# Kernel optimization log

Hardware: AMD Instinct MI355X
Metric: run time of the kernel (lower is better)

The kernel has to match this reference:

```python
import jax, jax.numpy as jnp
import numpy as np

B, L, DIM, H = 2, 2048, 2048, 16
D = DIM // H  # head_dim = 128
EPS = 1e-6


def _rope_freqs(seq_len: int, head_dim: int, theta: float = 10000.0) -> jnp.ndarray:
    # Flux-style rotation matrix: [1, 1, L, D/2, 2, 2]
    pos = np.arange(seq_len, dtype=np.float32)
    inv = 1.0 / (theta ** (np.arange(0, head_dim, 2, dtype=np.float32) / head_dim))
    ang = np.einsum('l,d->ld', pos, inv)  # [L, D/2]
    cos, sin = np.cos(ang), np.sin(ang)
    rot = np.stack([np.stack([cos, -sin], -1), np.stack([sin, cos], -1)], -2)  # [L, D/2, 2, 2]
    return jnp.asarray(rot[None, None])


def _rms_norm(x, scale):
    rrms = jax.lax.rsqrt(jnp.mean(jnp.square(x), axis=-1, keepdims=True) + EPS)
    return x * rrms * scale


def _apply_rope(xq, xk, freqs_cis):
    # xq/xk: [B, H, L, D]; freqs_cis: [1, 1, L, D/2, 2, 2]
    def rot(x):
        xr = x.reshape(*x.shape[:-1], -1, 1, 2)  # [B,H,L,D/2,1,2]
        out = freqs_cis[..., 0] * xr[..., 0] + freqs_cis[..., 1] * xr[..., 1]
        return out.reshape(x.shape)
    return rot(xq), rot(xk)


def setup_inputs() -> dict:
    key = jax.random.key(0)
    ks = jax.random.split(key, 4)
    x = jax.random.normal(ks[0], (B, L, DIM), dtype=jnp.float32)
    qkv_w = jax.random.normal(ks[1], (DIM, 3 * DIM), dtype=jnp.float32) * 0.02
    qkv_b = jnp.zeros((3 * DIM,), dtype=jnp.float32)
    q_scale = jnp.ones((D,), dtype=jnp.float32)
    k_scale = jnp.ones((D,), dtype=jnp.float32)
    proj_w = jax.random.normal(ks[2], (DIM, DIM), dtype=jnp.float32) * 0.02
    proj_b = jnp.zeros((DIM,), dtype=jnp.float32)
    pe = _rope_freqs(L, D)
    return {"x": x, "pe": pe, "qkv_w": qkv_w, "qkv_b": qkv_b,
            "q_scale": q_scale, "k_scale": k_scale,
            "proj_w": proj_w, "proj_b": proj_b}


def reference(x, pe, qkv_w, qkv_b, q_scale, k_scale, proj_w, proj_b):
    b, l, _ = x.shape
    qkv = x @ qkv_w + qkv_b                      # [B, L, 3*DIM]
    qkv = qkv.reshape(b, l, 3, H, D)
    qkv = jnp.transpose(qkv, (2, 0, 3, 1, 4))    # [3, B, H, L, D]
    q, k, v = qkv[0], qkv[1], qkv[2]
    q = _rms_norm(q, q_scale)
    k = _rms_norm(k, k_scale)
    q, k = _apply_rope(q, k, pe)
    scores = jnp.einsum('bhqd,bhkd->bhqk', q, k) / jnp.sqrt(jnp.float32(D))
    attn = jax.nn.softmax(scores, axis=-1)
    o = jnp.einsum('bhqk,bhkd->bhqd', attn, v)   # [B, H, L, D]
    o = jnp.transpose(o, (0, 2, 1, 3)).reshape(b, l, H * D)
    return o @ proj_w + proj_b
```

## Files before the change

### kernel.cpp

```cpp
#include <hip/hip_runtime.h>
#include <cstdint>
#include <cstddef>

#define BB 2
#define HB 16
#define LL 2048
#define DD 128
#define MM 4096
#define KK 2048
#define N1 6144
#define N2 2048
#define BHLD (BB*HB*LL*DD)

typedef unsigned short u16;
typedef __bf16 bf16x8 __attribute__((ext_vector_type(8)));
typedef short  s16x4  __attribute__((ext_vector_type(4)));
typedef float  f32x4  __attribute__((ext_vector_type(4)));

typedef __attribute__((address_space(1))) void* as1_ptr;
typedef __attribute__((address_space(3))) void* as3_ptr;

__device__ __forceinline__ void gload16(const void* g, void* l) {
  __builtin_amdgcn_global_load_lds((as1_ptr)g, (as3_ptr)l, 16, 0, 0);
}

__device__ __forceinline__ float bf2f(u16 u) {
  union { unsigned v; float f; } c; c.v = ((unsigned)u) << 16; return c.f;
}
__device__ __forceinline__ u16 f2bf(float f) {
  unsigned u = __builtin_bit_cast(unsigned, f);
  return (u16)((u + 0x7FFFu + ((u >> 16) & 1u)) >> 16);
}


__global__ __launch_bounds__(256) void f32_to_bf16_vec(
    const float* __restrict__ in, u16* __restrict__ out, int n4) {
  int i = blockIdx.x * 256 + threadIdx.x;
  if (i >= n4) return;
  float4 v = ((const float4*)in)[i];
  ushort4 o;
  o.x = f2bf(v.x); o.y = f2bf(v.y); o.z = f2bf(v.z); o.w = f2bf(v.w);
  ((ushort4*)out)[i] = o;
}

__global__ __launch_bounds__(256) void transpose_f32_bf16(
    const float* __restrict__ in, u16* __restrict__ out, int R, int C) {
  __shared__ float t[32][33];
  int c0 = blockIdx.x * 32, r0 = blockIdx.y * 32;
  int tx = threadIdx.x & 31, ty = threadIdx.x >> 5;
#pragma unroll
  for (int i = ty; i < 32; i += 8)
    t[i][tx] = in[(size_t)(r0 + i) * C + c0 + tx];
  __syncthreads();
#pragma unroll
  for (int i = ty; i < 32; i += 8)
    out[(size_t)(c0 + i) * R + r0 + tx] = f2bf(t[tx][i]);
}

template<int MODE>
__global__ __launch_bounds__(256) void gemm_bt(
    const u16* __restrict__ A, const u16* __restrict__ Bt,
    const float* __restrict__ bias, void* __restrict__ Cout,
    int Msz, int Nsz, int Ksz)
{
  __shared__ __align__(16) u16 As[128*64];
  __shared__ __align__(16) u16 Bs[128*64];
  const int tid  = threadIdx.x;
  const int lane = tid & 63;
  const int wid  = tid >> 6;
  const int l15  = lane & 15, quad = lane >> 4;
  const int m0 = blockIdx.y * 128, n0 = blockIdx.x * 128;
  const int wm = (wid >> 1) * 64, wn = (wid & 1) * 64;

  f32x4 acc[4][4] = {};

  for (int ks = 0; ks < Ksz; ks += 64) {
    __syncthreads();
#pragma unroll
    for (int j = 0; j < 4; j++) {
      const int s = (wid*4 + j)*64 + lane;
      const int row = s >> 3, pc = (s & 7) ^ (row & 7);
      gload16(&A [(size_t)(m0 + row) * Ksz + ks + pc*8], &As[(wid*4 + j)*512]);
      gload16(&Bt[(size_t)(n0 + row) * Ksz + ks + pc*8], &Bs[(wid*4 + j)*512]);
    }
    __syncthreads();
#pragma unroll
    for (int kh = 0; kh < 2; kh++) {
      bf16x8 af[4], bfr[4];
#pragma unroll
      for (int i = 0; i < 4; i++) {
        const int r = wm + i*16 + l15;
        af[i]  = *(const bf16x8*)&As[r*64 + (((kh*4 + quad) ^ (r & 7)))*8];
      }
#pragma unroll
      for (int i = 0; i < 4; i++) {
        const int r = wn + i*16 + l15;
        bfr[i] = *(const bf16x8*)&Bs[r*64 + (((kh*4 + quad) ^ (r & 7)))*8];
      }
#pragma unroll
      for (int i = 0; i < 4; i++)
#pragma unroll
        for (int j = 0; j < 4; j++)
          acc[i][j] = __builtin_amdgcn_mfma_f32_16x16x32_bf16(af[i], bfr[j], acc[i][j], 0, 0, 0);
    }
  }

#pragma unroll
  for (int i = 0; i < 4; i++) {
#pragma unroll
    for (int j = 0; j < 4; j++) {
      const int col = n0 + wn + j*16 + l15;
      const float bv = bias[col];
#pragma unroll
      for (int r = 0; r < 4; r++) {
        const int row = m0 + wm + i*16 + quad*4 + r;
        float v = acc[i][j][r] + bv;
        if (MODE == 0) {
          u16* qkv = (u16*)Cout;
          int t = col >> 11, hd = col & 2047, h = hd >> 7, d = hd & 127;
          int b = row >> 11, l = row & (LL - 1);
          size_t dst;
          if (t < 2) dst = (size_t)t * BHLD + (((size_t)(b*HB + h)) * LL + l) * DD + d;
          else       dst = (size_t)2 * BHLD + (((size_t)(b*HB + h)) * DD + d) * LL + l;
          qkv[dst] = f2bf(v);
        } else {
          ((float*)Cout)[(size_t)row * Nsz + col] = v;
        }
      }
    }
  }
}

__global__ __launch_bounds__(256) void norm_rope(
    u16* __restrict__ qkv, const float* __restrict__ pe,
    const float* __restrict__ qsc, const float* __restrict__ ksc)
{
  const int wid = threadIdx.x >> 6, lane = threadIdx.x & 63;
  const int r = blockIdx.x * 4 + wid;
  const int l = r & (LL - 1);
  const float4 p4 = *(const float4*)&pe[((size_t)l * 64 + lane) * 4];
#pragma unroll
  for (int t = 0; t < 2; t++) {
    u16* base = qkv + (size_t)t * BHLD + (size_t)r * DD + lane * 2;
    const float* sc = t ? ksc : qsc;
    ushort2 xx = *(const ushort2*)base;
    float x0 = bf2f(xx.x), x1 = bf2f(xx.y);
    float ss = x0*x0 + x1*x1;
#pragma unroll
    for (int m = 1; m < 64; m <<= 1) ss += __shfl_xor(ss, m, 64);
    float rr = rsqrtf(ss * (1.0f/128.0f) + 1e-6f);
    if (t == 0) rr *= 0.08838834764831845f;
    float y0 = x0 * rr * sc[lane*2], y1 = x1 * rr * sc[lane*2 + 1];
    ushort2 oo;
    oo.x = f2bf(p4.x * y0 + p4.y * y1);
    oo.y = f2bf(p4.z * y0 + p4.w * y1);
    *(ushort2*)base = oo;
  }
}

#define BKT 64
__global__ __launch_bounds__(256, 2) void attn(
    const u16* __restrict__ qkv, u16* __restrict__ Oout)
{
  __shared__ __align__(16) u16 Ksh[2][BKT * DD];
  __shared__ __align__(16) u16 Vsh[2][DD * BKT];

  const int bh = blockIdx.x >> 4, qt = blockIdx.x & 15;
  const int wid = threadIdx.x >> 6, lane = threadIdx.x & 63;
  const int l15 = lane & 15, quad = lane >> 4;
  const int q0 = qt * 128 + wid * 32;
  const u16* qp = qkv + (size_t)bh * LL * DD;
  const u16* kp = qkv + (size_t)BHLD + (size_t)bh * LL * DD;
  const u16* vp = qkv + (size_t)2 * BHLD + (size_t)bh * DD * LL;

  bf16x8 qb[2][4];
#pragma unroll
  for (int qf = 0; qf < 2; qf++)
#pragma unroll
    for (int f = 0; f < 4; f++)
      qb[qf][f] = *(const bf16x8*)&qp[(size_t)(q0 + qf*16 + l15) * DD + f*32 + quad*8];

  float l_acc[2] = {0.f, 0.f};
  f32x4 oacc[2][8] = {};

  auto stage = [&](int buf, int k0) {
#pragma unroll
    for (int j = 0; j < 4; j++) {
      const int s = (wid*4 + j)*64 + lane;
      {
        const int r = s >> 4, c = s & 15;
        const int lc = (c & 8) | ((c & 7) ^ (r & 7));
        gload16(&kp[(size_t)(k0 + r) * DD + lc*8], &Ksh[buf][(wid*4 + j)*512]);
      }
      {
        const int r = s >> 3, c = s & 7;
        const int lc = c ^ (r & 7);
        gload16(&vp[(size_t)r * LL + k0 + lc*8], &Vsh[buf][(wid*4 + j)*512]);
      }
    }
  };

  stage(0, 0);
  int cur = 0;

  for (int k0 = 0; k0 < LL; k0 += BKT) {
    __syncthreads();
    if (k0 + BKT < LL) stage(cur ^ 1, k0 + BKT);

    f32x4 s[2][4] = {};
#pragma unroll
    for (int f = 0; f < 4; f++) {
      bf16x8 kf[4];
#pragma unroll
      for (int mt = 0; mt < 4; mt++) {
        const int rr = mt*16 + l15;
        const int Lc = f*4 + quad;
        const int pc = (Lc & 8) | ((Lc & 7) ^ (rr & 7));
        kf[mt] = *(const bf16x8*)&Ksh[cur][rr*DD + pc*8];
      }
#pragma unroll
      for (int qf = 0; qf < 2; qf++)
#pragma unroll
        for (int mt = 0; mt < 4; mt++)
          s[qf][mt] = __builtin_amdgcn_mfma_f32_16x16x32_bf16(kf[mt], qb[qf][f], s[qf][mt], 0, 0, 0);
    }

    s16x4 pa[2][4];
#pragma unroll
    for (int qf = 0; qf < 2; qf++) {
#pragma unroll
      for (int mt = 0; mt < 4; mt++) {
        float p0 = __expf(s[qf][mt][0] - 12.f);
        float p1 = __expf(s[qf][mt][1] - 12.f);
        float p2 = __expf(s[qf][mt][2] - 12.f);
        float p3 = __expf(s[qf][mt][3] - 12.f);
        l_acc[qf] += (p0 + p1) + (p2 + p3);
        pa[qf][mt][0] = (short)f2bf(p0); pa[qf][mt][1] = (short)f2bf(p1);
        pa[qf][mt][2] = (short)f2bf(p2); pa[qf][mt][3] = (short)f2bf(p3);
      }
    }

#pragma unroll
    for (int t = 0; t < 4; t++) {
      s16x4 vb[8];
#pragma unroll
      for (int c = 0; c < 8; c++) {
        const int rv = c*16 + l15;
        const int pc = (t*2 + (quad >> 1)) ^ (l15 & 7);
        vb[c] = *(const s16x4*)&Vsh[cur][rv*BKT + pc*8 + (quad & 1)*4];
      }
#pragma unroll
      for (int qf = 0; qf < 2; qf++)
#pragma unroll
        for (int c = 0; c < 8; c++)
          oacc[qf][c] = __builtin_amdgcn_mfma_f32_16x16x16bf16_1k(pa[qf][t], vb[c], oacc[qf][c], 0, 0, 0);
    }
    cur ^= 1;
  }

#pragma unroll
  for (int qf = 0; qf < 2; qf++) {
    l_acc[qf] += __shfl_xor(l_acc[qf], 16, 64);
    l_acc[qf] += __shfl_xor(l_acc[qf], 32, 64);
  }
  const int b = bh >> 4, h = bh & 15;
#pragma unroll
  for (int qf = 0; qf < 2; qf++) {
    float lr[4];
#pragma unroll
    for (int r = 0; r < 4; r++)
      lr[r] = 1.0f / __shfl(l_acc[qf], (quad << 4) | (quad*4 + r), 64);
#pragma unroll
    for (int c = 0; c < 8; c++)
#pragma unroll
      for (int r = 0; r < 4; r++) {
        int qrow = q0 + qf*16 + quad*4 + r;
        Oout[((size_t)(b*LL + qrow)) * N2 + h*DD + c*16 + l15] = f2bf(oacc[qf][c][r] * lr[r]);
      }
  }
}


extern "C" void kernel_launch(void* const* d_in, const int* in_sizes, int n_in,
                              void* d_out, int out_size, void* d_ws, size_t ws_size,
                              hipStream_t stream) {
  const float* x       = (const float*)d_in[0];
  const float* pe      = (const float*)d_in[1];
  const float* qkv_w   = (const float*)d_in[2];
  const float* qkv_b   = (const float*)d_in[3];
  const float* q_scale = (const float*)d_in[4];
  const float* k_scale = (const float*)d_in[5];
  const float* proj_w  = (const float*)d_in[6];
  const float* proj_b  = (const float*)d_in[7];

  char* ws = (char*)d_ws;
  u16* xb   = (u16*)(ws + 0);
  u16* w1t  = (u16*)(ws + 16777216);
  u16* w2t  = (u16*)(ws + 41943040);
  u16* qkv  = (u16*)(ws + 50331648);
  u16* attO = (u16*)(ws + 100663296);

  f32_to_bf16_vec<<<(MM*KK/4)/256, 256, 0, stream>>>(x, xb, MM*KK/4);
  transpose_f32_bf16<<<dim3(N1/32, KK/32), 256, 0, stream>>>(qkv_w, w1t, KK, N1);
  transpose_f32_bf16<<<dim3(N2/32, KK/32), 256, 0, stream>>>(proj_w, w2t, KK, N2);
  gemm_bt<0><<<dim3(N1/128, MM/128), 256, 0, stream>>>(xb, w1t, qkv_b, (void*)qkv, MM, N1, KK);
  norm_rope<<<(BB*HB*LL)/4, 256, 0, stream>>>(qkv, pe, q_scale, k_scale);
  attn<<<BB*HB*(LL/128), 256, 0, stream>>>(qkv, attO);
  gemm_bt<1><<<dim3(N2/128, MM/128), 256, 0, stream>>>(attO, w2t, proj_b, d_out, MM, N2, KK);
}
```

Measured before the change: 435.6 us.

## Replace GEMM with 256x256 double-buffered 8-wave pipelined kernel

Replaces the 128x128 single-buffered bf16 GEMM with a 256x256 tile, 512-thread kernel that double-buffers A/B in LDS and interleaves global-to-LDS loads with MFMA phases, using barriers, waitcnt and setprio. It also remaps workgroup indices with a swizzle so neighbouring blocks are spread out, aimed at L2 locality. The goal is to hide global load latency and raise data reuse per block. In exchange it uses 128KB of LDS per block and many more accumulator registers. The 2048x2048 projection GEMM then has only 128 blocks, which may underfill the GPU.

```diff
diff --git a/kernel.cpp b/kernel.cpp
--- a/kernel.cpp
+++ b/kernel.cpp
@@ -57,72 +57,133 @@
     out[(size_t)(c0 + i) * R + r0 + tx] = f2bf(t[tx][i]);
 }
 
+
+#define PH_ENTER \
+  __builtin_amdgcn_s_barrier(); \
+  asm volatile("s_waitcnt lgkmcnt(0)" ::: "memory"); \
+  __builtin_amdgcn_sched_barrier(0); \
+  __builtin_amdgcn_s_setprio(1);
+#define PH_EXIT \
+  __builtin_amdgcn_s_setprio(0); \
+  __builtin_amdgcn_s_barrier();
+#define PH_EXIT_VM \
+  __builtin_amdgcn_s_setprio(0); \
+  asm volatile("s_waitcnt vmcnt(4)" ::: "memory"); \
+  __builtin_amdgcn_s_barrier();
+
+#define QUAD_MFMA(MB, NB) \
+  { _Pragma("unroll") for (int mm = 0; mm < 4; mm++) \
+    _Pragma("unroll") for (int nn = 0; nn < 2; nn++) { \
+      acc[(MB)+mm][(NB)+nn] = __builtin_amdgcn_mfma_f32_16x16x32_bf16(af[mm][0], bfr[(NB)+nn][0], acc[(MB)+mm][(NB)+nn], 0, 0, 0); \
+      acc[(MB)+mm][(NB)+nn] = __builtin_amdgcn_mfma_f32_16x16x32_bf16(af[mm][1], bfr[(NB)+nn][1], acc[(MB)+mm][(NB)+nn], 0, 0, 0); \
+    } }
+
+#define LOAD_A4(BSEL, MH) \
+  { _Pragma("unroll") for (int mm = 0; mm < 4; mm++) \
+    _Pragma("unroll") for (int ks = 0; ks < 2; ks++) { \
+      const int r_ = wr*128 + ((MH)*4 + mm)*16 + l15; \
+      af[mm][ks] = *(const bf16x8*)&As[BSEL][r_*64 + (((ks*4 + quad) ^ (r_ & 7)) << 3)]; \
+    } }
+#define LOAD_B2(BSEL, NB) \
+  { _Pragma("unroll") for (int nn = 0; nn < 2; nn++) \
+    _Pragma("unroll") for (int ks = 0; ks < 2; ks++) { \
+      const int r_ = wc*64 + ((NB) + nn)*16 + l15; \
+      bfr[(NB)+nn][ks] = *(const bf16x8*)&Bs[BSEL][r_*64 + (((ks*4 + quad) ^ (r_ & 7)) << 3)]; \
+    } }
+
 template<int MODE>
-__global__ __launch_bounds__(256) void gemm_bt(
-    const u16* __restrict__ A, const u16* __restrict__ Bt,
+__global__ __launch_bounds__(512, 2) void gemm256(
+    const u16* __restrict__ Ag, const u16* __restrict__ Bg,
     const float* __restrict__ bias, void* __restrict__ Cout,
     int Msz, int Nsz, int Ksz)
 {
-  __shared__ __align__(16) u16 As[128*64];
-  __shared__ __align__(16) u16 Bs[128*64];
+  __shared__ __align__(16) u16 As[2][256*64];
+  __shared__ __align__(16) u16 Bs[2][256*64];
+
   const int tid  = threadIdx.x;
   const int lane = tid & 63;
   const int wid  = tid >> 6;
   const int l15  = lane & 15, quad = lane >> 4;
-  const int m0 = blockIdx.y * 128, n0 = blockIdx.x * 128;
-  const int wm = (wid >> 1) * 64, wn = (wid & 1) * 64;
-
-  f32x4 acc[4][4] = {};
-
-  for (int ks = 0; ks < Ksz; ks += 64) {
-    __syncthreads();
-#pragma unroll
-    for (int j = 0; j < 4; j++) {
-      const int s = (wid*4 + j)*64 + lane;
-      const int row = s >> 3, pc = (s & 7) ^ (row & 7);
-      gload16(&A [(size_t)(m0 + row) * Ksz + ks + pc*8], &As[(wid*4 + j)*512]);
-      gload16(&Bt[(size_t)(n0 + row) * Ksz + ks + pc*8], &Bs[(wid*4 + j)*512]);
-    }
-    __syncthreads();
-#pragma unroll
-    for (int kh = 0; kh < 2; kh++) {
-      bf16x8 af[4], bfr[4];
-#pragma unroll
-      for (int i = 0; i < 4; i++) {
-        const int r = wm + i*16 + l15;
-        af[i]  = *(const bf16x8*)&As[r*64 + (((kh*4 + quad) ^ (r & 7)))*8];
-      }
-#pragma unroll
-      for (int i = 0; i < 4; i++) {
-        const int r = wn + i*16 + l15;
-        bfr[i] = *(const bf16x8*)&Bs[r*64 + (((kh*4 + quad) ^ (r & 7)))*8];
-      }
-#pragma unroll
-      for (int i = 0; i < 4; i++)
-#pragma unroll
-        for (int j = 0; j < 4; j++)
-          acc[i][j] = __builtin_amdgcn_mfma_f32_16x16x32_bf16(af[i], bfr[j], acc[i][j], 0, 0, 0);
-    }
-  }
-
-#pragma unroll
-  for (int i = 0; i < 4; i++) {
-#pragma unroll
-    for (int j = 0; j < 4; j++) {
-      const int col = n0 + wn + j*16 + l15;
+  const int wr   = wid >> 2, wc = wid & 3;
+
+  const int nwg = gridDim.x * gridDim.y;
+  const int lin = blockIdx.y * gridDim.x + blockIdx.x;
+  const int swz = (lin & 7) * (nwg >> 3) + (lin >> 3);
+  const int bn0 = (swz % gridDim.x) * 256;
+  const int bm0 = (swz / gridDim.x) * 256;
+
+  f32x4 acc[8][4] = {};
+  bf16x8 af[4][2], bfr[4][2];
+
+  auto stageA = [&](int bsel, int h, int k0) {
+#pragma unroll
+    for (int j = 0; j < 2; j++) {
+      const int s = j*512 + tid;
+      const int r = s >> 3, c = s & 7;
+      gload16(&Ag[(size_t)(bm0 + h*128 + r) * Ksz + k0 + ((c ^ (r & 7)) << 3)],
+              &As[bsel][h*8192 + (j*512 + wid*64)*8]);
+    }
+  };
+  auto stageB = [&](int bsel, int h, int k0) {
+#pragma unroll
+    for (int j = 0; j < 2; j++) {
+      const int s = j*512 + tid;
+      const int r = s >> 3, c = s & 7;
+      gload16(&Bg[(size_t)(bn0 + h*128 + r) * Ksz + k0 + ((c ^ (r & 7)) << 3)],
+              &Bs[bsel][h*8192 + (j*512 + wid*64)*8]);
+    }
+  };
+
+  stageB(0, 0, 0); stageB(0, 1, 0);
+  stageA(0, 0, 0); stageA(0, 1, 0);
+  stageB(1, 0, 64); stageB(1, 1, 64);
+  asm volatile("s_waitcnt vmcnt(4)" ::: "memory");
+  __builtin_amdgcn_s_barrier();
+
+  const int niter = Ksz >> 7;
+#pragma unroll 1
+  for (int it = 0; it < niter; it++) {
+    const int t1 = it*128 + 64;
+    int t2 = it*128 + 128; if (t2 >= Ksz) t2 -= Ksz;
+    int t3 = it*128 + 192; if (t3 >= Ksz) t3 -= Ksz;
+
+    LOAD_A4(0, 0); LOAD_B2(0, 0); stageA(1, 0, t1);
+    PH_ENTER; QUAD_MFMA(0, 0); PH_EXIT;
+    LOAD_B2(0, 2); stageA(1, 1, t1);
+    PH_ENTER; QUAD_MFMA(0, 2); PH_EXIT;
+    LOAD_A4(0, 1); stageB(0, 0, t2);
+    PH_ENTER; QUAD_MFMA(4, 0); PH_EXIT;
+    stageB(0, 1, t2);
+    PH_ENTER; QUAD_MFMA(4, 2); PH_EXIT_VM;
+
+    LOAD_A4(1, 0); LOAD_B2(1, 0); stageA(0, 0, t2);
+    PH_ENTER; QUAD_MFMA(0, 0); PH_EXIT;
+    LOAD_B2(1, 2); stageA(0, 1, t2);
+    PH_ENTER; QUAD_MFMA(0, 2); PH_EXIT;
+    LOAD_A4(1, 1); stageB(1, 0, t3);
+    PH_ENTER; QUAD_MFMA(4, 0); PH_EXIT;
+    stageB(1, 1, t3);
+    PH_ENTER; QUAD_MFMA(4, 2); PH_EXIT_VM;
+  }
+
+#pragma unroll
+  for (int m = 0; m < 8; m++) {
+#pragma unroll
+    for (int n = 0; n < 4; n++) {
+      const int col = bn0 + wc*64 + n*16 + l15;
       const float bv = bias[col];
 #pragma unroll
-      for (int r = 0; r < 4; r++) {
-        const int row = m0 + wm + i*16 + quad*4 + r;
-        float v = acc[i][j][r] + bv;
+      for (int rr = 0; rr < 4; rr++) {
+        const int row = bm0 + wr*128 + m*16 + quad*4 + rr;
+        float v = acc[m][n][rr] + bv;
         if (MODE == 0) {
-          u16* qkv = (u16*)Cout;
-          int t = col >> 11, hd = col & 2047, h = hd >> 7, d = hd & 127;
+          u16* qkvp = (u16*)Cout;
+          int t = col >> 11, hd = col & 2047, hh = hd >> 7, d = hd & 127;
           int b = row >> 11, l = row & (LL - 1);
           size_t dst;
-          if (t < 2) dst = (size_t)t * BHLD + (((size_t)(b*HB + h)) * LL + l) * DD + d;
-          else       dst = (size_t)2 * BHLD + (((size_t)(b*HB + h)) * DD + d) * LL + l;
-          qkv[dst] = f2bf(v);
+          if (t < 2) dst = (size_t)t * BHLD + (((size_t)(b*HB + hh)) * LL + l) * DD + d;
+          else       dst = (size_t)2 * BHLD + (((size_t)(b*HB + hh)) * DD + d) * LL + l;
+          qkvp[dst] = f2bf(v);
         } else {
           ((float*)Cout)[(size_t)row * Nsz + col] = v;
         }
@@ -303,8 +364,8 @@
   f32_to_bf16_vec<<<(MM*KK/4)/256, 256, 0, stream>>>(x, xb, MM*KK/4);
   transpose_f32_bf16<<<dim3(N1/32, KK/32), 256, 0, stream>>>(qkv_w, w1t, KK, N1);
   transpose_f32_bf16<<<dim3(N2/32, KK/32), 256, 0, stream>>>(proj_w, w2t, KK, N2);
-  gemm_bt<0><<<dim3(N1/128, MM/128), 256, 0, stream>>>(xb, w1t, qkv_b, (void*)qkv, MM, N1, KK);
+  gemm256<0><<<dim3(N1/256, MM/256), 512, 0, stream>>>(xb, w1t, qkv_b, (void*)qkv, MM, N1, KK);
   norm_rope<<<(BB*HB*LL)/4, 256, 0, stream>>>(qkv, pe, q_scale, k_scale);
   attn<<<BB*HB*(LL/128), 256, 0, stream>>>(qkv, attO);
-  gemm_bt<1><<<dim3(N2/128, MM/128), 256, 0, stream>>>(attO, w2t, proj_b, d_out, MM, N2, KK);
-}
+  gemm256<1><<<dim3(N2/256, MM/256), 512, 0, stream>>>(attO, w2t, proj_b, d_out, MM, N2, KK);
+}
```

New measurement: 475.5 us. 1.09x slower.

## Fuse RMSNorm and RoPE into QKV GEMM epilogue, add MFMA priority hints

Applied to the files above, without the earlier changes.

The QKV GEMM epilogue now computes per-row RMS norms across the 128-wide head tile, using shuffles plus a small shared-memory reduction between the two column warps. It then applies the scale and the rotary rotation, pairing elements with a lane xor shuffle, before writing Q and K. This removes the separate norm_rope kernel and its read-modify-write pass over Q and K. The attention kernel also wraps its MFMA blocks in s_setprio and uses the native bf16 conversion for P. The cost is a heavier GEMM epilogue with an extra barrier and scattered pe loads.

```diff
diff --git a/kernel.cpp b/kernel.cpp
--- a/kernel.cpp
+++ b/kernel.cpp
@@ -61,10 +61,13 @@
 __global__ __launch_bounds__(256) void gemm_bt(
     const u16* __restrict__ A, const u16* __restrict__ Bt,
     const float* __restrict__ bias, void* __restrict__ Cout,
+    const float* __restrict__ pe, const float* __restrict__ qsc,
+    const float* __restrict__ ksc,
     int Msz, int Nsz, int Ksz)
 {
   __shared__ __align__(16) u16 As[128*64];
   __shared__ __align__(16) u16 Bs[128*64];
+  __shared__ float red[128][2];
   const int tid  = threadIdx.x;
   const int lane = tid & 63;
   const int wid  = tid >> 6;
@@ -105,56 +108,80 @@
     }
   }
 
-#pragma unroll
-  for (int i = 0; i < 4; i++) {
-#pragma unroll
-    for (int j = 0; j < 4; j++) {
-      const int col = n0 + wn + j*16 + l15;
-      const float bv = bias[col];
-#pragma unroll
-      for (int r = 0; r < 4; r++) {
-        const int row = m0 + wm + i*16 + quad*4 + r;
-        float v = acc[i][j][r] + bv;
-        if (MODE == 0) {
-          u16* qkv = (u16*)Cout;
-          int t = col >> 11, hd = col & 2047, h = hd >> 7, d = hd & 127;
-          int b = row >> 11, l = row & (LL - 1);
-          size_t dst;
-          if (t < 2) dst = (size_t)t * BHLD + (((size_t)(b*HB + h)) * LL + l) * DD + d;
-          else       dst = (size_t)2 * BHLD + (((size_t)(b*HB + h)) * DD + d) * LL + l;
-          qkv[dst] = f2bf(v);
-        } else {
-          ((float*)Cout)[(size_t)row * Nsz + col] = v;
+  if (MODE == 0) {
+    u16* qkvp = (u16*)Cout;
+    const int t = n0 >> 11;
+    const int hh = (n0 & 2047) >> 7;
+#pragma unroll
+    for (int i = 0; i < 4; i++)
+#pragma unroll
+      for (int j = 0; j < 4; j++) {
+        const float bv = bias[n0 + wn + j*16 + l15];
+#pragma unroll
+        for (int r = 0; r < 4; r++) acc[i][j][r] += bv;
+      }
+
+    if (t == 2) {
+#pragma unroll
+      for (int i = 0; i < 4; i++)
+#pragma unroll
+        for (int j = 0; j < 4; j++) {
+          const int d = wn + j*16 + l15;
+#pragma unroll
+          for (int r = 0; r < 4; r++) {
+            const int row = m0 + wm + i*16 + quad*4 + r;
+            const int b = row >> 11, l = row & (LL - 1);
+            qkvp[(size_t)2 * BHLD + (((size_t)(b*HB + hh)) * DD + d) * LL + l] =
+                f2bf(acc[i][j][r]);
+          }
         }
-      }
-    }
-  }
-}
-
-__global__ __launch_bounds__(256) void norm_rope(
-    u16* __restrict__ qkv, const float* __restrict__ pe,
-    const float* __restrict__ qsc, const float* __restrict__ ksc)
-{
-  const int wid = threadIdx.x >> 6, lane = threadIdx.x & 63;
-  const int r = blockIdx.x * 4 + wid;
-  const int l = r & (LL - 1);
-  const float4 p4 = *(const float4*)&pe[((size_t)l * 64 + lane) * 4];
-#pragma unroll
-  for (int t = 0; t < 2; t++) {
-    u16* base = qkv + (size_t)t * BHLD + (size_t)r * DD + lane * 2;
-    const float* sc = t ? ksc : qsc;
-    ushort2 xx = *(const ushort2*)base;
-    float x0 = bf2f(xx.x), x1 = bf2f(xx.y);
-    float ss = x0*x0 + x1*x1;
-#pragma unroll
-    for (int m = 1; m < 64; m <<= 1) ss += __shfl_xor(ss, m, 64);
-    float rr = rsqrtf(ss * (1.0f/128.0f) + 1e-6f);
-    if (t == 0) rr *= 0.08838834764831845f;
-    float y0 = x0 * rr * sc[lane*2], y1 = x1 * rr * sc[lane*2 + 1];
-    ushort2 oo;
-    oo.x = f2bf(p4.x * y0 + p4.y * y1);
-    oo.y = f2bf(p4.z * y0 + p4.w * y1);
-    *(ushort2*)base = oo;
+    } else {
+      const float* sc = (t == 0) ? qsc : ksc;
+#pragma unroll
+      for (int i = 0; i < 4; i++)
+#pragma unroll
+        for (int r = 0; r < 4; r++) {
+          float s2 = 0.f;
+#pragma unroll
+          for (int j = 0; j < 4; j++) { const float v = acc[i][j][r]; s2 += v * v; }
+#pragma unroll
+          for (int m = 1; m < 16; m <<= 1) s2 += __shfl_xor(s2, m, 64);
+          if (l15 == 0) red[wm + i*16 + quad*4 + r][wid & 1] = s2;
+        }
+      __syncthreads();
+#pragma unroll
+      for (int i = 0; i < 4; i++)
+#pragma unroll
+        for (int r = 0; r < 4; r++) {
+          const int rowl = wm + i*16 + quad*4 + r;
+          const float tot = red[rowl][0] + red[rowl][1];
+          float rr = rsqrtf(tot * (1.0f/128.0f) + 1e-6f);
+          if (t == 0) rr *= 0.08838834764831845f;
+          const int row = m0 + rowl, b = row >> 11, l = row & (LL - 1);
+#pragma unroll
+          for (int j = 0; j < 4; j++) {
+            const int d = wn + j*16 + l15;
+            const float y = acc[i][j][r] * rr * sc[d];
+            const float p = __shfl_xor(y, 1, 64);
+            const float2 pp = *(const float2*)&pe[(size_t)l * 256 + (d >> 1) * 4 + (d & 1) * 2];
+            const float o = pp.x * ((d & 1) ? p : y) + pp.y * ((d & 1) ? y : p);
+            qkvp[(size_t)t * BHLD + (((size_t)(b*HB + hh)) * LL + l) * DD + d] = f2bf(o);
+          }
+        }
+    }
+  } else {
+#pragma unroll
+    for (int i = 0; i < 4; i++)
+#pragma unroll
+      for (int j = 0; j < 4; j++) {
+        const int col = n0 + wn + j*16 + l15;
+        const float bv = bias[col];
+#pragma unroll
+        for (int r = 0; r < 4; r++) {
+          const int row = m0 + wm + i*16 + quad*4 + r;
+          ((float*)Cout)[(size_t)row * Nsz + col] = acc[i][j][r] + bv;
+        }
+      }
   }
 }
 
@@ -218,11 +245,13 @@
         const int pc = (Lc & 8) | ((Lc & 7) ^ (rr & 7));
         kf[mt] = *(const bf16x8*)&Ksh[cur][rr*DD + pc*8];
       }
+      __builtin_amdgcn_s_setprio(1);
 #pragma unroll
       for (int qf = 0; qf < 2; qf++)
 #pragma unroll
         for (int mt = 0; mt < 4; mt++)
           s[qf][mt] = __builtin_amdgcn_mfma_f32_16x16x32_bf16(kf[mt], qb[qf][f], s[qf][mt], 0, 0, 0);
+      __builtin_amdgcn_s_setprio(0);
     }
 
     s16x4 pa[2][4];
@@ -235,8 +264,10 @@
         float p2 = __expf(s[qf][mt][2] - 12.f);
         float p3 = __expf(s[qf][mt][3] - 12.f);
         l_acc[qf] += (p0 + p1) + (p2 + p3);
-        pa[qf][mt][0] = (short)f2bf(p0); pa[qf][mt][1] = (short)f2bf(p1);
-        pa[qf][mt][2] = (short)f2bf(p2); pa[qf][mt][3] = (short)f2bf(p3);
+        pa[qf][mt][0] = __builtin_bit_cast(short, (__bf16)p0);
+        pa[qf][mt][1] = __builtin_bit_cast(short, (__bf16)p1);
+        pa[qf][mt][2] = __builtin_bit_cast(short, (__bf16)p2);
+        pa[qf][mt][3] = __builtin_bit_cast(short, (__bf16)p3);
       }
     }
 
@@ -249,11 +280,13 @@
         const int pc = (t*2 + (quad >> 1)) ^ (l15 & 7);
         vb[c] = *(const s16x4*)&Vsh[cur][rv*BKT + pc*8 + (quad & 1)*4];
       }
+      __builtin_amdgcn_s_setprio(1);
 #pragma unroll
       for (int qf = 0; qf < 2; qf++)
 #pragma unroll
         for (int c = 0; c < 8; c++)
           oacc[qf][c] = __builtin_amdgcn_mfma_f32_16x16x16bf16_1k(pa[qf][t], vb[c], oacc[qf][c], 0, 0, 0);
+      __builtin_amdgcn_s_setprio(0);
     }
     cur ^= 1;
   }
@@ -303,8 +336,9 @@
   f32_to_bf16_vec<<<(MM*KK/4)/256, 256, 0, stream>>>(x, xb, MM*KK/4);
   transpose_f32_bf16<<<dim3(N1/32, KK/32), 256, 0, stream>>>(qkv_w, w1t, KK, N1);
   transpose_f32_bf16<<<dim3(N2/32, KK/32), 256, 0, stream>>>(proj_w, w2t, KK, N2);
-  gemm_bt<0><<<dim3(N1/128, MM/128), 256, 0, stream>>>(xb, w1t, qkv_b, (void*)qkv, MM, N1, KK);
-  norm_rope<<<(BB*HB*LL)/4, 256, 0, stream>>>(qkv, pe, q_scale, k_scale);
+  gemm_bt<0><<<dim3(N1/128, MM/128), 256, 0, stream>>>(
+      xb, w1t, qkv_b, (void*)qkv, pe, q_scale, k_scale, MM, N1, KK);
   attn<<<BB*HB*(LL/128), 256, 0, stream>>>(qkv, attO);
-  gemm_bt<1><<<dim3(N2/128, MM/128), 256, 0, stream>>>(attO, w2t, proj_b, d_out, MM, N2, KK);
-}
+  gemm_bt<1><<<dim3(N2/128, MM/128), 256, 0, stream>>>(
+      attO, w2t, proj_b, d_out, nullptr, nullptr, nullptr, MM, N2, KK);
+}
```

Measured after the change: 424.0 us. 2.7% less time.
